# Kernel tuning notes

Measured on AMD Instinct MI355X. Metric: run time of the kernel, lower is better.

Reference implementation:

```python
import jax, jax.numpy as jnp
import numpy as np


def deform_conv2d(x, w, offset, mask, pad):
    """Modulated deformable conv (DCNv2), stride 1, dilation 1, groups 1.
    x: [B,C,H,W], w: [Co,C,kh,kw], offset: [B,2*K,H,W] (y,x per tap), mask: [B,K,H,W].
    Output spatial size equals input (pad = (k-1)//2).
    """
    B, C, H, W = x.shape
    Co, _, kh, kw = w.shape
    K = kh * kw
    off = offset.reshape(B, K, 2, H, W)
    dy, dx = off[:, :, 0], off[:, :, 1]               # [B,K,H,W]
    ky, kx = jnp.meshgrid(jnp.arange(kh), jnp.arange(kw), indexing='ij')
    ky = ky.reshape(K).astype(x.dtype)
    kx = kx.reshape(K).astype(x.dtype)
    hh = jnp.arange(H, dtype=x.dtype)
    ww = jnp.arange(W, dtype=x.dtype)
    # sampling coords: p0 + p_k + delta p_k
    py = hh[None, None, :, None] - pad + ky[None, :, None, None] + dy  # [B,K,H,W]
    px = ww[None, None, None, :] - pad + kx[None, :, None, None] + dx
    y0 = jnp.floor(py)
    x0 = jnp.floor(px)
    wy = py - y0
    wx = px - x0
    y0i = y0.astype(jnp.int32)
    x0i = x0.astype(jnp.int32)
    x_flat = x.reshape(B, C, H * W)

    def gather(yi, xi):
        valid = (yi >= 0) & (yi < H) & (xi >= 0) & (xi < W)  # zero padding outside
        idx = jnp.clip(yi, 0, H - 1) * W + jnp.clip(xi, 0, W - 1)
        g = jnp.take_along_axis(x_flat, idx.reshape(B, 1, K * H * W), axis=2)
        g = g.reshape(B, C, K, H, W)
        return g * valid[:, None].astype(x.dtype)

    v00 = gather(y0i, x0i)
    v01 = gather(y0i, x0i + 1)
    v10 = gather(y0i + 1, x0i)
    v11 = gather(y0i + 1, x0i + 1)
    wy_ = wy[:, None]  # [B,1,K,H,W]
    wx_ = wx[:, None]
    samp = (v00 * (1 - wy_) * (1 - wx_) + v01 * (1 - wy_) * wx_
            + v10 * wy_ * (1 - wx_) + v11 * wy_ * wx_)   # [B,C,K,H,W]
    # masked weighted accumulation == conv over sampled taps
    return jnp.einsum('bckhw,bkhw,ock->bohw', samp, mask, w.reshape(Co, C, K))


def setup_inputs() -> dict:
    key = jax.random.key(0)
    ks = jax.random.split(key, 10)
    B, C, H, W, Co = 4, 64, 64, 64, 64
    inp = {
        'x': jax.random.normal(ks[0], (B, C, H, W), dtype=jnp.float32),
        'filter1': jax.random.normal(ks[1], (Co, C, 3, 3), dtype=jnp.float32) * 0.05,
        'offset1': jax.random.normal(ks[2], (B, 2 * 9, H, W), dtype=jnp.float32),
        'mask1': jax.random.uniform(ks[3], (B, 9, H, W), dtype=jnp.float32),
        'filter2': jax.random.normal(ks[4], (Co, C, 5, 5), dtype=jnp.float32) * 0.03,
        'offset2': jax.random.normal(ks[5], (B, 2 * 25, H, W), dtype=jnp.float32),
        'mask2': jax.random.uniform(ks[6], (B, 25, H, W), dtype=jnp.float32),
        'filter3': jax.random.normal(ks[7], (Co, C, 7, 7), dtype=jnp.float32) * 0.02,
        'offset3': jax.random.normal(ks[8], (B, 2 * 49, H, W), dtype=jnp.float32),
        'mask3': jax.random.uniform(ks[9], (B, 49, H, W), dtype=jnp.float32),
    }
    return inp


def reference(x, filter1, offset1, mask1, filter2, offset2, mask2, filter3, offset3, mask3):
    part1 = deform_conv2d(x, filter1, offset1, mask1, pad=1)  # 3x3
    part2 = deform_conv2d(x, filter2, offset2, mask2, pad=2)  # 5x5
    part3 = deform_conv2d(x, filter3, offset3, mask3, pad=3)  # 7x7
    return jnp.concatenate((part1, part2, part3), axis=1)
```

## Files before the change

### kernel.cpp

```cpp
#include <hip/hip_runtime.h>
#include <hip/hip_bf16.h>


typedef __attribute__((ext_vector_type(8))) short bf16x8;
typedef __attribute__((ext_vector_type(8))) unsigned short u16x8;
typedef __attribute__((ext_vector_type(4))) float f32x4;
typedef __attribute__((ext_vector_type(2))) float f32x2;

#define SLS 20

__device__ __forceinline__ unsigned short f2bf(float f) {
    __hip_bfloat16 h = __float2bfloat16(f);
    return *reinterpret_cast<unsigned short*>(&h);
}
__device__ __forceinline__ f32x2 unpk(unsigned u) {
    f32x2 r;
    r[0] = __uint_as_float(u << 16);
    r[1] = __uint_as_float(u & 0xffff0000u);
    return r;
}

__global__ __launch_bounds__(256) void k_prep(
    const float* __restrict__ x,
    const float* __restrict__ f1, const float* __restrict__ f2, const float* __restrict__ f3,
    unsigned short* __restrict__ xTb,
    unsigned short* __restrict__ wp1, unsigned short* __restrict__ wp2, unsigned short* __restrict__ wp3) {
    __shared__ float tile[64][65];
    int bid = blockIdx.x;
    int tid = threadIdx.x;
    if (bid < 256) {
        int b = bid >> 6, h = bid & 63;
        {
            int w = tid & 63, c4 = tid >> 6;
            const float* xp = x + (((b * 64) * 64 + h) * 64) + w;
            #pragma unroll
            for (int i = 0; i < 16; ++i) {
                int c = c4 * 16 + i;
                tile[c][w] = xp[c * 4096];
            }
        }
        __syncthreads();
        {
            int c = tid & 63, w4 = tid >> 6;
            unsigned short* op = xTb + (((b * 64 + h) * 64) * 64) + c;
            #pragma unroll
            for (int i = 0; i < 16; ++i) {
                int ww = w4 * 16 + i;
                op[ww * 64] = f2bf(tile[c][ww]);
            }
        }
    } else {
        int idx = (bid - 256) * 256 + tid;
        const float* f; unsigned short* wp; int K, rel;
        if (idx < 36864)       { f = f1; wp = wp1; K = 9;  rel = idx; }
        else if (idx < 139264) { f = f2; wp = wp2; K = 25; rel = idx - 36864; }
        else                   { f = f3; wp = wp3; K = 49; rel = idx - 139264; }
        int k    = rel >> 12;
        int r2   = rel & 4095;
        int ct   = r2 >> 10;
        int cg   = (r2 >> 9) & 1;
        int lane = (r2 >> 3) & 63;
        int j    = r2 & 7;
        int o = ct * 16 + (lane & 15);
        int c = cg * 32 + (lane >> 4) * 8 + j;
        wp[rel] = f2bf(f[(o * 64 + c) * K + k]);
    }
}

__global__ __launch_bounds__(512, 4) void k_dcn(
    const unsigned short* __restrict__ xTb,
    const float* __restrict__ off1, const float* __restrict__ msk1, const unsigned short* __restrict__ wp1,
    const float* __restrict__ off2, const float* __restrict__ msk2, const unsigned short* __restrict__ wp2,
    const float* __restrict__ off3, const float* __restrict__ msk3, const unsigned short* __restrict__ wp3,
    float* __restrict__ out) {

    __shared__ __align__(16) float slab[8 * 1280];

    int tile = blockIdx.x;
    int b  = tile >> 8;
    int h  = (tile >> 2) & 63;
    int w0 = (tile & 3) << 4;

    int tid  = threadIdx.x;
    int wv   = tid >> 6;
    int lane = tid & 63;
    int quad = lane >> 4;
    int l16  = lane & 15;

    const unsigned short* xb = xTb + ((size_t)b << 18);

    int pw   = w0 + l16;
    int ch0  = quad << 3;
    int lofs = lane << 3;

    const float* offs; const float* msks; const unsigned short* wpF;
    int ks, ke, kw, pad;
    switch (wv) {
        case 0:  offs = off1; msks = msk1; wpF = wp1; kw = 3; pad = 1; ks = 0;  ke = 9;  break;
        case 1:  offs = off2; msks = msk2; wpF = wp2; kw = 5; pad = 2; ks = 0;  ke = 12; break;
        case 2:  offs = off2; msks = msk2; wpF = wp2; kw = 5; pad = 2; ks = 12; ke = 25; break;
        case 3:  offs = off3; msks = msk3; wpF = wp3; kw = 7; pad = 3; ks = 0;  ke = 10; break;
        case 4:  offs = off3; msks = msk3; wpF = wp3; kw = 7; pad = 3; ks = 10; ke = 20; break;
        case 5:  offs = off3; msks = msk3; wpF = wp3; kw = 7; pad = 3; ks = 20; ke = 30; break;
        case 6:  offs = off3; msks = msk3; wpF = wp3; kw = 7; pad = 3; ks = 30; ke = 40; break;
        default: offs = off3; msks = msk3; wpF = wp3; kw = 7; pad = 3; ks = 40; ke = 49; break;
    }
    int K2 = (kw == 3) ? 9 : (kw == 5) ? 25 : 49;
    const float* offp = offs + ((b * 2 * K2) * 4096) + (h << 6) + pw;
    const float* mskp = msks + ((b * K2) * 4096) + (h << 6) + pw;

    int kp1 = min(ks + 1, ke - 1), kp2 = min(ks + 2, ke - 1);
    float dyA = offp[ks * 8192], dxA = offp[ks * 8192 + 4096], mkA = mskp[ks * 4096];
    float dyB = offp[kp1 * 8192], dxB = offp[kp1 * 8192 + 4096], mkB = mskp[kp1 * 4096];
    float dyC = offp[kp2 * 8192], dxC = offp[kp2 * 8192 + 4096], mkC = mskp[kp2 * 4096];

    f32x4 acc[4];
    #pragma unroll
    for (int i = 0; i < 4; ++i) acc[i] = (f32x4){0.f, 0.f, 0.f, 0.f};

    int ky = ks / kw, kx = ks - ky * kw;

    for (int k = ks; k < ke; ++k) {
        const unsigned short* wpk = wpF + (k << 12) + lofs;
        bf16x8 b00 = *(const bf16x8*)(wpk);
        bf16x8 b01 = *(const bf16x8*)(wpk + 512);
        bf16x8 b10 = *(const bf16x8*)(wpk + 1024);
        bf16x8 b11 = *(const bf16x8*)(wpk + 1536);
        bf16x8 b20 = *(const bf16x8*)(wpk + 2048);
        bf16x8 b21 = *(const bf16x8*)(wpk + 2560);
        bf16x8 b30 = *(const bf16x8*)(wpk + 3072);
        bf16x8 b31 = *(const bf16x8*)(wpk + 3584);

        int kn = min(k + 3, ke - 1);
        float dyN = offp[kn * 8192];
        float dxN = offp[kn * 8192 + 4096];
        float mkN = mskp[kn * 4096];

        float py = (float)(h - pad + ky) + dyA;
        float px = (float)(pw - pad + kx) + dxA;
        float y0f = floorf(py), x0f = floorf(px);
        float wy = py - y0f, wx = px - x0f;
        int y0 = (int)y0f, x0 = (int)x0f;
        int y1 = y0 + 1, x1 = x0 + 1;
        float fy0 = ((unsigned)y0 < 64u) ? (1.f - wy) * mkA : 0.f;
        float fy1 = ((unsigned)y1 < 64u) ? wy * mkA         : 0.f;
        float gx0 = ((unsigned)x0 < 64u) ? (1.f - wx)       : 0.f;
        float gx1 = ((unsigned)x1 < 64u) ? wx               : 0.f;
        float w00 = fy0 * gx0, w01 = fy0 * gx1, w10 = fy1 * gx0, w11 = fy1 * gx1;

        int y0g = min(max(y0, 0), 63), y1g = min(max(y1, 0), 63);
        int x0g = min(max(x0, 0), 63), x1g = min(max(x1, 0), 63);
        int o00 = ((y0g << 6) + x0g) << 6;
        int o01 = ((y0g << 6) + x1g) << 6;
        int o10 = ((y1g << 6) + x0g) << 6;
        int o11 = ((y1g << 6) + x1g) << 6;

        union U { u16x8 v; unsigned u[4]; };
        U g00a, g01a, g10a, g11a, g00b, g01b, g10b, g11b;
        g00a.v = *(const u16x8*)(xb + o00 + ch0);
        g01a.v = *(const u16x8*)(xb + o01 + ch0);
        g10a.v = *(const u16x8*)(xb + o10 + ch0);
        g11a.v = *(const u16x8*)(xb + o11 + ch0);
        g00b.v = *(const u16x8*)(xb + o00 + 32 + ch0);
        g01b.v = *(const u16x8*)(xb + o01 + 32 + ch0);
        g10b.v = *(const u16x8*)(xb + o10 + 32 + ch0);
        g11b.v = *(const u16x8*)(xb + o11 + 32 + ch0);

        f32x2 W00 = {w00, w00}, W01 = {w01, w01}, W10 = {w10, w10}, W11 = {w11, w11};
        union { bf16x8 v; unsigned short u[8]; } A0, A1;
        #pragma unroll
        for (int j2 = 0; j2 < 4; ++j2) {
            f32x2 s0 = W00 * unpk(g00a.u[j2]) + W01 * unpk(g01a.u[j2])
                     + W10 * unpk(g10a.u[j2]) + W11 * unpk(g11a.u[j2]);
            f32x2 s1 = W00 * unpk(g00b.u[j2]) + W01 * unpk(g01b.u[j2])
                     + W10 * unpk(g10b.u[j2]) + W11 * unpk(g11b.u[j2]);
            A0.u[2 * j2]     = f2bf(s0[0]);
            A0.u[2 * j2 + 1] = f2bf(s0[1]);
            A1.u[2 * j2]     = f2bf(s1[0]);
            A1.u[2 * j2 + 1] = f2bf(s1[1]);
        }

        acc[0] = __builtin_amdgcn_mfma_f32_16x16x32_bf16(A0.v, b00, acc[0], 0, 0, 0);
        acc[0] = __builtin_amdgcn_mfma_f32_16x16x32_bf16(A1.v, b01, acc[0], 0, 0, 0);
        acc[1] = __builtin_amdgcn_mfma_f32_16x16x32_bf16(A0.v, b10, acc[1], 0, 0, 0);
        acc[1] = __builtin_amdgcn_mfma_f32_16x16x32_bf16(A1.v, b11, acc[1], 0, 0, 0);
        acc[2] = __builtin_amdgcn_mfma_f32_16x16x32_bf16(A0.v, b20, acc[2], 0, 0, 0);
        acc[2] = __builtin_amdgcn_mfma_f32_16x16x32_bf16(A1.v, b21, acc[2], 0, 0, 0);
        acc[3] = __builtin_amdgcn_mfma_f32_16x16x32_bf16(A0.v, b30, acc[3], 0, 0, 0);
        acc[3] = __builtin_amdgcn_mfma_f32_16x16x32_bf16(A1.v, b31, acc[3], 0, 0, 0);

        dyA = dyB; dyB = dyC; dyC = dyN;
        dxA = dxB; dxB = dxC; dxC = dxN;
        mkA = mkB; mkB = mkC; mkC = mkN;
        if (++kx == kw) { kx = 0; ++ky; }
    }

    #pragma unroll
    for (int ct = 0; ct < 4; ++ct) {
        *(f32x4*)&slab[wv * 1280 + (ct * 16 + l16) * SLS + quad * 4] = acc[ct];
    }
    __syncthreads();

    for (int it = tid; it < 768; it += 512) {
        int g = it & 3;
        int o = it >> 2;
        int oo = o & 63;
        int base = oo * SLS + g * 4;
        f32x4 v;
        if (o < 64) {
            v = *(const f32x4*)&slab[base];
        } else if (o < 128) {
            f32x4 a0 = *(const f32x4*)&slab[1 * 1280 + base];
            f32x4 a1 = *(const f32x4*)&slab[2 * 1280 + base];
            #pragma unroll
            for (int r = 0; r < 4; ++r) v[r] = a0[r] + a1[r];
        } else {
            f32x4 a0 = *(const f32x4*)&slab[3 * 1280 + base];
            f32x4 a1 = *(const f32x4*)&slab[4 * 1280 + base];
            f32x4 a2 = *(const f32x4*)&slab[5 * 1280 + base];
            f32x4 a3 = *(const f32x4*)&slab[6 * 1280 + base];
            f32x4 a4 = *(const f32x4*)&slab[7 * 1280 + base];
            #pragma unroll
            for (int r = 0; r < 4; ++r) v[r] = (a0[r] + a1[r]) + (a2[r] + a3[r]) + a4[r];
        }
        *(f32x4*)&out[(((size_t)b * 192 + o) * 64 + h) * 64 + w0 + g * 4] = v;
    }
}

extern "C" void kernel_launch(void* const* d_in, const int* in_sizes, int n_in,
                              void* d_out, int out_size, void* d_ws, size_t ws_size,
                              hipStream_t stream) {
    const float* x    = (const float*)d_in[0];
    const float* f1   = (const float*)d_in[1];
    const float* off1 = (const float*)d_in[2];
    const float* msk1 = (const float*)d_in[3];
    const float* f2   = (const float*)d_in[4];
    const float* off2 = (const float*)d_in[5];
    const float* msk2 = (const float*)d_in[6];
    const float* f3   = (const float*)d_in[7];
    const float* off3 = (const float*)d_in[8];
    const float* msk3 = (const float*)d_in[9];
    float* out = (float*)d_out;

    unsigned short* xTb = (unsigned short*)d_ws;
    unsigned short* wp1 = xTb + 4 * 64 * 64 * 64;
    unsigned short* wp2 = wp1 + 9 * 4096;
    unsigned short* wp3 = wp2 + 25 * 4096;

    k_prep<<<dim3(1584), dim3(256), 0, stream>>>(x, f1, f2, f3, xTb, wp1, wp2, wp3);
    k_dcn<<<dim3(1024), dim3(512), 0, stream>>>(xTb,
                                                off1, msk1, wp1,
                                                off2, msk2, wp2,
                                                off3, msk3, wp3,
                                                out);
}
```

Measured before the change: 176.0 us.

## Stage 2D input halo window in LDS and compute two pixel sets per wave

Each block now covers a 4x8 pixel tile instead of a 1x16 row, and first stages an 18x22-pixel bf16 channels-last halo window of the input into shared memory. Bilinear taps are then read from LDS, falling back to global memory only when a sample lands outside the window. Each wave processes two 16-pixel sets, so every weight fragment loaded feeds twice as many MFMAs. The accumulator reduction is split into two passes through a reused LDS buffer. In exchange, occupancy drops (launch bounds go from 4 to 2 blocks, about 54KB of LDS per block), there are only 512 blocks, and register pressure rises from the doubled accumulators and the shallower offset prefetch.

Result: faster. 170.9 us (-2.9%).

```diff
diff --git a/kernel.cpp b/kernel.cpp
--- a/kernel.cpp
+++ b/kernel.cpp
@@ -7,7 +7,10 @@
 typedef __attribute__((ext_vector_type(4))) float f32x4;
 typedef __attribute__((ext_vector_type(2))) float f32x2;
 
-#define SLS 20
+#define WR 18
+#define WC 22
+#define WS 68
+#define SLS2 36
 
 __device__ __forceinline__ unsigned short f2bf(float f) {
     __hip_bfloat16 h = __float2bfloat16(f);
@@ -67,29 +70,100 @@
     }
 }
 
-__global__ __launch_bounds__(512, 4) void k_dcn(
+#define PIXSET(S, ph_, pw_, dy_, dx_, mk_)                                    \
+    {                                                                         \
+        float py = (float)((ph_) - pad + ky) + (dy_);                         \
+        float px = (float)((pw_) - pad + kx) + (dx_);                         \
+        float y0f = floorf(py), x0f = floorf(px);                             \
+        float wy = py - y0f, wx = px - x0f;                                   \
+        int y0 = (int)y0f, x0 = (int)x0f;                                     \
+        int y1 = y0 + 1, x1 = x0 + 1;                                         \
+        float fy0 = ((unsigned)y0 < 64u) ? (1.f - wy) * (mk_) : 0.f;          \
+        float fy1 = ((unsigned)y1 < 64u) ? wy * (mk_)         : 0.f;          \
+        float gx0 = ((unsigned)x0 < 64u) ? (1.f - wx)         : 0.f;          \
+        float gx1 = ((unsigned)x1 < 64u) ? wx                 : 0.f;          \
+        float w00 = fy0 * gx0, w01 = fy0 * gx1;                               \
+        float w10 = fy1 * gx0, w11 = fy1 * gx1;                               \
+        int r0 = y0 - ylo, r1 = r0 + 1;                                       \
+        int c0 = x0 - cxlo, c1 = c0 + 1;                                      \
+        bool oow = ((w00 != 0.f) & (((unsigned)r0 >= WR) | ((unsigned)c0 >= WC)))  \
+                 | ((w01 != 0.f) & (((unsigned)r0 >= WR) | ((unsigned)c1 >= WC)))  \
+                 | ((w10 != 0.f) & (((unsigned)r1 >= WR) | ((unsigned)c0 >= WC)))  \
+                 | ((w11 != 0.f) & (((unsigned)r1 >= WR) | ((unsigned)c1 >= WC))); \
+        int r0c = min(max(r0, 0), WR - 1), r1c = min(max(r1, 0), WR - 1);     \
+        int c0c = min(max(c0, 0), WC - 1), c1c = min(max(c1, 0), WC - 1);     \
+        int p00 = (r0c * WC + c0c) * WS;                                      \
+        int p01 = (r0c * WC + c1c) * WS;                                      \
+        int p10 = (r1c * WC + c0c) * WS;                                      \
+        int p11 = (r1c * WC + c1c) * WS;                                      \
+        union U { u16x8 v; unsigned u[4]; };                                  \
+        U g00a, g01a, g10a, g11a, g00b, g01b, g10b, g11b;                     \
+        g00a.v = *(const u16x8*)(win + p00 + ch0);                            \
+        g01a.v = *(const u16x8*)(win + p01 + ch0);                            \
+        g10a.v = *(const u16x8*)(win + p10 + ch0);                            \
+        g11a.v = *(const u16x8*)(win + p11 + ch0);                            \
+        g00b.v = *(const u16x8*)(win + p00 + 32 + ch0);                       \
+        g01b.v = *(const u16x8*)(win + p01 + 32 + ch0);                       \
+        g10b.v = *(const u16x8*)(win + p10 + 32 + ch0);                       \
+        g11b.v = *(const u16x8*)(win + p11 + 32 + ch0);                       \
+        if (oow) {                                                            \
+            int y0g = min(max(y0, 0), 63), y1g = min(max(y1, 0), 63);         \
+            int x0g = min(max(x0, 0), 63), x1g = min(max(x1, 0), 63);         \
+            int o00 = ((y0g << 6) + x0g) << 6;                                \
+            int o01 = ((y0g << 6) + x1g) << 6;                                \
+            int o10 = ((y1g << 6) + x0g) << 6;                                \
+            int o11 = ((y1g << 6) + x1g) << 6;                                \
+            g00a.v = *(const u16x8*)(xb + o00 + ch0);                         \
+            g01a.v = *(const u16x8*)(xb + o01 + ch0);                         \
+            g10a.v = *(const u16x8*)(xb + o10 + ch0);                         \
+            g11a.v = *(const u16x8*)(xb + o11 + ch0);                         \
+            g00b.v = *(const u16x8*)(xb + o00 + 32 + ch0);                    \
+            g01b.v = *(const u16x8*)(xb + o01 + 32 + ch0);                    \
+            g10b.v = *(const u16x8*)(xb + o10 + 32 + ch0);                    \
+            g11b.v = *(const u16x8*)(xb + o11 + 32 + ch0);                    \
+        }                                                                     \
+        f32x2 W00 = {w00, w00}, W01 = {w01, w01};                             \
+        f32x2 W10 = {w10, w10}, W11 = {w11, w11};                             \
+        _Pragma("unroll")                                                     \
+        for (int j2 = 0; j2 < 4; ++j2) {                                      \
+            f32x2 s0 = W00 * unpk(g00a.u[j2]) + W01 * unpk(g01a.u[j2])        \
+                     + W10 * unpk(g10a.u[j2]) + W11 * unpk(g11a.u[j2]);       \
+            f32x2 s1 = W00 * unpk(g00b.u[j2]) + W01 * unpk(g01b.u[j2])        \
+                     + W10 * unpk(g10b.u[j2]) + W11 * unpk(g11b.u[j2]);       \
+            A0##S.u[2 * j2]     = f2bf(s0[0]);                                \
+            A0##S.u[2 * j2 + 1] = f2bf(s0[1]);                                \
+            A1##S.u[2 * j2]     = f2bf(s1[0]);                                \
+            A1##S.u[2 * j2 + 1] = f2bf(s1[1]);                                \
+        }                                                                     \
+    }
+
+__global__ __launch_bounds__(512, 2) void k_dcn(
     const unsigned short* __restrict__ xTb,
     const float* __restrict__ off1, const float* __restrict__ msk1, const unsigned short* __restrict__ wp1,
     const float* __restrict__ off2, const float* __restrict__ msk2, const unsigned short* __restrict__ wp2,
     const float* __restrict__ off3, const float* __restrict__ msk3, const unsigned short* __restrict__ wp3,
     float* __restrict__ out) {
 
-    __shared__ __align__(16) float slab[8 * 1280];
+    __shared__ __align__(16) unsigned char smem[WR * WC * WS * 2];
+    unsigned short* win = (unsigned short*)smem;
+    float* slab = (float*)smem;
 
     int tile = blockIdx.x;
-    int b  = tile >> 8;
-    int h  = (tile >> 2) & 63;
-    int w0 = (tile & 3) << 4;
+    int b  = tile >> 7;
+    int h0 = ((tile >> 3) & 15) << 2;
+    int w0 = (tile & 7) << 3;
 
     int tid  = threadIdx.x;
     int wv   = tid >> 6;
     int lane = tid & 63;
     int quad = lane >> 4;
     int l16  = lane & 15;
+    int ylo  = h0 - 7, cxlo = w0 - 7;
 
     const unsigned short* xb = xTb + ((size_t)b << 18);
 
-    int pw   = w0 + l16;
+    int phA = h0 + (l16 >> 3),     pwA = w0 + (l16 & 7);
+    int phB = h0 + 2 + (l16 >> 3), pwB = w0 + (l16 & 7);
     int ch0  = quad << 3;
     int lofs = lane << 3;
 
@@ -106,17 +180,32 @@
         default: offs = off3; msks = msk3; wpF = wp3; kw = 7; pad = 3; ks = 40; ke = 49; break;
     }
     int K2 = (kw == 3) ? 9 : (kw == 5) ? 25 : 49;
-    const float* offp = offs + ((b * 2 * K2) * 4096) + (h << 6) + pw;
-    const float* mskp = msks + ((b * K2) * 4096) + (h << 6) + pw;
-
-    int kp1 = min(ks + 1, ke - 1), kp2 = min(ks + 2, ke - 1);
-    float dyA = offp[ks * 8192], dxA = offp[ks * 8192 + 4096], mkA = mskp[ks * 4096];
-    float dyB = offp[kp1 * 8192], dxB = offp[kp1 * 8192 + 4096], mkB = mskp[kp1 * 4096];
-    float dyC = offp[kp2 * 8192], dxC = offp[kp2 * 8192 + 4096], mkC = mskp[kp2 * 4096];
-
-    f32x4 acc[4];
+    const float* offpA = offs + ((b * 2 * K2) * 4096) + (phA << 6) + pwA;
+    const float* mskpA = msks + ((b * K2) * 4096) + (phA << 6) + pwA;
+    const float* offpB = offs + ((b * 2 * K2) * 4096) + (phB << 6) + pwB;
+    const float* mskpB = msks + ((b * K2) * 4096) + (phB << 6) + pwB;
+
+    float dyCa = offpA[ks * 8192], dxCa = offpA[ks * 8192 + 4096], mkCa = mskpA[ks * 4096];
+    float dyCb = offpB[ks * 8192], dxCb = offpB[ks * 8192 + 4096], mkCb = mskpB[ks * 4096];
+
+    {
+        int j = tid & 7;
+        for (int p = tid >> 3; p < WR * WC; p += 64) {
+            int r = p / WC, cc = p - r * WC;
+            int y = min(max(ylo + r, 0), 63);
+            int x = min(max(cxlo + cc, 0), 63);
+            *(u16x8*)(win + p * WS + j * 8) =
+                *(const u16x8*)(xb + (((y << 6) + x) << 6) + j * 8);
+        }
+    }
+    __syncthreads();
+
+    f32x4 accA[4], accB[4];
     #pragma unroll
-    for (int i = 0; i < 4; ++i) acc[i] = (f32x4){0.f, 0.f, 0.f, 0.f};
+    for (int i = 0; i < 4; ++i) {
+        accA[i] = (f32x4){0.f, 0.f, 0.f, 0.f};
+        accB[i] = (f32x4){0.f, 0.f, 0.f, 0.f};
+    }
 
     int ky = ks / kw, kx = ks - ky * kw;
 
@@ -131,99 +220,83 @@
         bf16x8 b30 = *(const bf16x8*)(wpk + 3072);
         bf16x8 b31 = *(const bf16x8*)(wpk + 3584);
 
-        int kn = min(k + 3, ke - 1);
-        float dyN = offp[kn * 8192];
-        float dxN = offp[kn * 8192 + 4096];
-        float mkN = mskp[kn * 4096];
-
-        float py = (float)(h - pad + ky) + dyA;
-        float px = (float)(pw - pad + kx) + dxA;
-        float y0f = floorf(py), x0f = floorf(px);
-        float wy = py - y0f, wx = px - x0f;
-        int y0 = (int)y0f, x0 = (int)x0f;
-        int y1 = y0 + 1, x1 = x0 + 1;
-        float fy0 = ((unsigned)y0 < 64u) ? (1.f - wy) * mkA : 0.f;
-        float fy1 = ((unsigned)y1 < 64u) ? wy * mkA         : 0.f;
-        float gx0 = ((unsigned)x0 < 64u) ? (1.f - wx)       : 0.f;
-        float gx1 = ((unsigned)x1 < 64u) ? wx               : 0.f;
-        float w00 = fy0 * gx0, w01 = fy0 * gx1, w10 = fy1 * gx0, w11 = fy1 * gx1;
-
-        int y0g = min(max(y0, 0), 63), y1g = min(max(y1, 0), 63);
-        int x0g = min(max(x0, 0), 63), x1g = min(max(x1, 0), 63);
-        int o00 = ((y0g << 6) + x0g) << 6;
-        int o01 = ((y0g << 6) + x1g) << 6;
-        int o10 = ((y1g << 6) + x0g) << 6;
-        int o11 = ((y1g << 6) + x1g) << 6;
-
-        union U { u16x8 v; unsigned u[4]; };
-        U g00a, g01a, g10a, g11a, g00b, g01b, g10b, g11b;
-        g00a.v = *(const u16x8*)(xb + o00 + ch0);
-        g01a.v = *(const u16x8*)(xb + o01 + ch0);
-        g10a.v = *(const u16x8*)(xb + o10 + ch0);
-        g11a.v = *(const u16x8*)(xb + o11 + ch0);
-        g00b.v = *(const u16x8*)(xb + o00 + 32 + ch0);
-        g01b.v = *(const u16x8*)(xb + o01 + 32 + ch0);
-        g10b.v = *(const u16x8*)(xb + o10 + 32 + ch0);
-        g11b.v = *(const u16x8*)(xb + o11 + 32 + ch0);
-
-        f32x2 W00 = {w00, w00}, W01 = {w01, w01}, W10 = {w10, w10}, W11 = {w11, w11};
-        union { bf16x8 v; unsigned short u[8]; } A0, A1;
+        int kn = min(k + 1, ke - 1);
+        float dyNa = offpA[kn * 8192], dxNa = offpA[kn * 8192 + 4096], mkNa = mskpA[kn * 4096];
+        float dyNb = offpB[kn * 8192], dxNb = offpB[kn * 8192 + 4096], mkNb = mskpB[kn * 4096];
+
+        union { bf16x8 v; unsigned short u[8]; } A0a, A1a, A0b, A1b;
+        PIXSET(a, phA, pwA, dyCa, dxCa, mkCa)
+        PIXSET(b, phB, pwB, dyCb, dxCb, mkCb)
+
+        accA[0] = __builtin_amdgcn_mfma_f32_16x16x32_bf16(A0a.v, b00, accA[0], 0, 0, 0);
+        accA[0] = __builtin_amdgcn_mfma_f32_16x16x32_bf16(A1a.v, b01, accA[0], 0, 0, 0);
+        accA[1] = __builtin_amdgcn_mfma_f32_16x16x32_bf16(A0a.v, b10, accA[1], 0, 0, 0);
+        accA[1] = __builtin_amdgcn_mfma_f32_16x16x32_bf16(A1a.v, b11, accA[1], 0, 0, 0);
+        accA[2] = __builtin_amdgcn_mfma_f32_16x16x32_bf16(A0a.v, b20, accA[2], 0, 0, 0);
+        accA[2] = __builtin_amdgcn_mfma_f32_16x16x32_bf16(A1a.v, b21, accA[2], 0, 0, 0);
+        accA[3] = __builtin_amdgcn_mfma_f32_16x16x32_bf16(A0a.v, b30, accA[3], 0, 0, 0);
+        accA[3] = __builtin_amdgcn_mfma_f32_16x16x32_bf16(A1a.v, b31, accA[3], 0, 0, 0);
+        accB[0] = __builtin_amdgcn_mfma_f32_16x16x32_bf16(A0b.v, b00, accB[0], 0, 0, 0);
+        accB[0] = __builtin_amdgcn_mfma_f32_16x16x32_bf16(A1b.v, b01, accB[0], 0, 0, 0);
+        accB[1] = __builtin_amdgcn_mfma_f32_16x16x32_bf16(A0b.v, b10, accB[1], 0, 0, 0);
+        accB[1] = __builtin_amdgcn_mfma_f32_16x16x32_bf16(A1b.v, b11, accB[1], 0, 0, 0);
+        accB[2] = __builtin_amdgcn_mfma_f32_16x16x32_bf16(A0b.v, b20, accB[2], 0, 0, 0);
+        accB[2] = __builtin_amdgcn_mfma_f32_16x16x32_bf16(A1b.v, b21, accB[2], 0, 0, 0);
+        accB[3] = __builtin_amdgcn_mfma_f32_16x16x32_bf16(A0b.v, b30, accB[3], 0, 0, 0);
+        accB[3] = __builtin_amdgcn_mfma_f32_16x16x32_bf16(A1b.v, b31, accB[3], 0, 0, 0);
+
+        dyCa = dyNa; dxCa = dxNa; mkCa = mkNa;
+        dyCb = dyNb; dxCb = dxNb; mkCb = mkNb;
+        if (++kx == kw) { kx = 0; ++ky; }
+    }
+
+    __syncthreads();
+
+    if (wv < 3) {
         #pragma unroll
-        for (int j2 = 0; j2 < 4; ++j2) {
-            f32x2 s0 = W00 * unpk(g00a.u[j2]) + W01 * unpk(g01a.u[j2])
-                     + W10 * unpk(g10a.u[j2]) + W11 * unpk(g11a.u[j2]);
-            f32x2 s1 = W00 * unpk(g00b.u[j2]) + W01 * unpk(g01b.u[j2])
-                     + W10 * unpk(g10b.u[j2]) + W11 * unpk(g11b.u[j2]);
-            A0.u[2 * j2]     = f2bf(s0[0]);
-            A0.u[2 * j2 + 1] = f2bf(s0[1]);
-            A1.u[2 * j2]     = f2bf(s1[0]);
-            A1.u[2 * j2 + 1] = f2bf(s1[1]);
-        }
-
-        acc[0] = __builtin_amdgcn_mfma_f32_16x16x32_bf16(A0.v, b00, acc[0], 0, 0, 0);
-        acc[0] = __builtin_amdgcn_mfma_f32_16x16x32_bf16(A1.v, b01, acc[0], 0, 0, 0);
-        acc[1] = __builtin_amdgcn_mfma_f32_16x16x32_bf16(A0.v, b10, acc[1], 0, 0, 0);
-        acc[1] = __builtin_amdgcn_mfma_f32_16x16x32_bf16(A1.v, b11, acc[1], 0, 0, 0);
-        acc[2] = __builtin_amdgcn_mfma_f32_16x16x32_bf16(A0.v, b20, acc[2], 0, 0, 0);
-        acc[2] = __builtin_amdgcn_mfma_f32_16x16x32_bf16(A1.v, b21, acc[2], 0, 0, 0);
-        acc[3] = __builtin_amdgcn_mfma_f32_16x16x32_bf16(A0.v, b30, acc[3], 0, 0, 0);
-        acc[3] = __builtin_amdgcn_mfma_f32_16x16x32_bf16(A1.v, b31, acc[3], 0, 0, 0);
-
-        dyA = dyB; dyB = dyC; dyC = dyN;
-        dxA = dxB; dxB = dxC; dxC = dxN;
-        mkA = mkB; mkB = mkC; mkC = mkN;
-        if (++kx == kw) { kx = 0; ++ky; }
-    }
-
-    #pragma unroll
-    for (int ct = 0; ct < 4; ++ct) {
-        *(f32x4*)&slab[wv * 1280 + (ct * 16 + l16) * SLS + quad * 4] = acc[ct];
-    }
-    __syncthreads();
-
-    for (int it = tid; it < 768; it += 512) {
-        int g = it & 3;
-        int o = it >> 2;
-        int oo = o & 63;
-        int base = oo * SLS + g * 4;
+        for (int ct = 0; ct < 4; ++ct) {
+            *(f32x4*)&slab[wv * 2304 + (ct * 16 + l16) * SLS2 + quad * 4]      = accA[ct];
+            *(f32x4*)&slab[wv * 2304 + (ct * 16 + l16) * SLS2 + 16 + quad * 4] = accB[ct];
+        }
+    }
+    __syncthreads();
+    for (int it = tid; it < 1024; it += 512) {
+        int o = it >> 3, grp = it & 7;
+        int base = (o & 63) * SLS2 + grp * 4;
         f32x4 v;
         if (o < 64) {
             v = *(const f32x4*)&slab[base];
-        } else if (o < 128) {
-            f32x4 a0 = *(const f32x4*)&slab[1 * 1280 + base];
-            f32x4 a1 = *(const f32x4*)&slab[2 * 1280 + base];
+        } else {
+            f32x4 a0 = *(const f32x4*)&slab[1 * 2304 + base];
+            f32x4 a1 = *(const f32x4*)&slab[2 * 2304 + base];
             #pragma unroll
             for (int r = 0; r < 4; ++r) v[r] = a0[r] + a1[r];
-        } else {
-            f32x4 a0 = *(const f32x4*)&slab[3 * 1280 + base];
-            f32x4 a1 = *(const f32x4*)&slab[4 * 1280 + base];
-            f32x4 a2 = *(const f32x4*)&slab[5 * 1280 + base];
-            f32x4 a3 = *(const f32x4*)&slab[6 * 1280 + base];
-            f32x4 a4 = *(const f32x4*)&slab[7 * 1280 + base];
-            #pragma unroll
-            for (int r = 0; r < 4; ++r) v[r] = (a0[r] + a1[r]) + (a2[r] + a3[r]) + a4[r];
-        }
-        *(f32x4*)&out[(((size_t)b * 192 + o) * 64 + h) * 64 + w0 + g * 4] = v;
+        }
+        *(f32x4*)&out[(((size_t)b * 192 + o) * 64 + h0 + (grp >> 1)) * 64 + w0 + (grp & 1) * 4] = v;
+    }
+    __syncthreads();
+
+    if (wv >= 3) {
+        #pragma unroll
+        for (int ct = 0; ct < 4; ++ct) {
+            *(f32x4*)&slab[(wv - 3) * 2304 + (ct * 16 + l16) * SLS2 + quad * 4]      = accA[ct];
+            *(f32x4*)&slab[(wv - 3) * 2304 + (ct * 16 + l16) * SLS2 + 16 + quad * 4] = accB[ct];
+        }
+    }
+    __syncthreads();
+    {
+        int it = tid;
+        int oo = it >> 3, grp = it & 7;
+        int base = oo * SLS2 + grp * 4;
+        f32x4 a0 = *(const f32x4*)&slab[0 * 2304 + base];
+        f32x4 a1 = *(const f32x4*)&slab[1 * 2304 + base];
+        f32x4 a2 = *(const f32x4*)&slab[2 * 2304 + base];
+        f32x4 a3 = *(const f32x4*)&slab[3 * 2304 + base];
+        f32x4 a4 = *(const f32x4*)&slab[4 * 2304 + base];
+        f32x4 v;
+        #pragma unroll
+        for (int r = 0; r < 4; ++r) v[r] = (a0[r] + a1[r]) + (a2[r] + a3[r]) + a4[r];
+        *(f32x4*)&out[(((size_t)b * 192 + 128 + oo) * 64 + h0 + (grp >> 1)) * 64 + w0 + (grp & 1) * 4] = v;
     }
 }
 
@@ -248,9 +321,9 @@
     unsigned short* wp3 = wp2 + 25 * 4096;
 
     k_prep<<<dim3(1584), dim3(256), 0, stream>>>(x, f1, f2, f3, xTb, wp1, wp2, wp3);
-    k_dcn<<<dim3(1024), dim3(512), 0, stream>>>(xTb,
-                                                off1, msk1, wp1,
-                                                off2, msk2, wp2,
-                                                off3, msk3, wp3,
-                                                out);
-}
+    k_dcn<<<dim3(512), dim3(512), 0, stream>>>(xTb,
+                                               off1, msk1, wp1,
+                                               off2, msk2, wp2,
+                                               off3, msk3, wp3,
+                                               out);
+}
```
